# Kernel tuning notes

Hardware: AMD Instinct MI355X
Metric: run time of the kernel (lower is better)

Reference implementation:

```python
import jax, jax.numpy as jnp
import numpy as np

N = 20000      # num_nodes
E = 320000     # num_edges (avg degree 16)
HID = 256      # hid_dim
H = 4          # attention heads
D = HID // H   # per-head dim (concat heads -> HID)
L = 2          # nGAT_layer
OUT = 12       # out_dim / pred_len (decoder steps)
NEG_SLOPE = 0.2


def setup_inputs() -> dict:
    key = jax.random.key(0)
    ks = jax.random.split(key, 16)
    s = 0.05
    nrm = lambda k, shape: jax.random.normal(k, shape, jnp.float32) * s
    return dict(
        x=nrm(ks[0], (N, HID)),
        edge_index=jax.random.randint(ks[1], (2, E), 0, N, dtype=jnp.int32),
        # GATv2Conv params per layer (stacked over L layers)
        gat_w_src=nrm(ks[2], (L, HID, H * D)),
        gat_w_dst=nrm(ks[3], (L, HID, H * D)),
        gat_att=nrm(ks[4], (L, H, D)),
        gat_bias=nrm(ks[5], (L, H * D)),
        # decoder_mlp: Linear(1 + HID -> HID)
        mlp_w=nrm(ks[6], (HID, 1 + HID)),
        mlp_b=nrm(ks[7], (HID,)),
        # nn.LSTM (1 layer, input HID, hidden HID), torch gate order i,f,g,o
        lstm_w_ih=nrm(ks[8], (4 * HID, HID)),
        lstm_w_hh=nrm(ks[9], (4 * HID, HID)),
        lstm_b_ih=nrm(ks[10], (4 * HID,)),
        lstm_b_hh=nrm(ks[11], (4 * HID,)),
        # decoder_init_proj: Linear(HID -> 1); decoder_output_proj: Linear(HID -> 1)
        init_w=nrm(ks[12], (1, HID)),
        init_b=nrm(ks[13], (1,)),
        out_w=nrm(ks[14], (1, HID)),
        out_b=nrm(ks[15], (1,)),
    )


def _gatv2_layer(x, src, dst, w_src, w_dst, att, bias):
    n = x.shape[0]
    xl = (x @ w_src).reshape(n, H, D)   # source-side projection
    xr = (x @ w_dst).reshape(n, H, D)   # destination-side projection
    # GATv2: e_ij = a^T LeakyReLU(Wl x_j + Wr x_i)
    e = jax.nn.leaky_relu(xl[src] + xr[dst], NEG_SLOPE)        # [E,H,D]
    logits = jnp.einsum('ehd,hd->eh', e, att)                   # [E,H]
    # edge softmax over incoming edges of each destination node
    m = jax.ops.segment_max(logits, dst, num_segments=n)        # [N,H]
    ex = jnp.exp(logits - m[dst])
    denom = jax.ops.segment_sum(ex, dst, num_segments=n)
    alpha = ex / denom[dst]                                     # [E,H]
    out = jax.ops.segment_sum(xl[src] * alpha[:, :, None], dst, num_segments=n)
    return out.reshape(n, H * D) + bias


def reference(x, edge_index, gat_w_src, gat_w_dst, gat_att, gat_bias,
              mlp_w, mlp_b, lstm_w_ih, lstm_w_hh, lstm_b_ih, lstm_b_hh,
              init_w, init_b, out_w, out_b):
    src, dst = edge_index[0], edge_index[1]
    # stacked GAT blocks: GATv2Conv + ELU (element == 2)
    for l in range(L):
        x = _gatv2_layer(x, src, dst, gat_w_src[l], gat_w_dst[l], gat_att[l], gat_bias[l])
        x = jax.nn.elu(x)
    # recurrent LSTM decoder, batch = nodes, seq step by step
    ctx = x                      # encoder_context
    h = x                        # h_0 = x (num_layers = 1)
    c = jnp.zeros_like(x)        # c_0 = 0
    prev = x @ init_w.T + init_b  # [N,1]
    outs = []
    for _ in range(OUT):
        dec_in = jnp.concatenate([prev, ctx], axis=1) @ mlp_w.T + mlp_b  # [N,HID]
        gates = dec_in @ lstm_w_ih.T + lstm_b_ih + h @ lstm_w_hh.T + lstm_b_hh
        i_g, f_g, g_g, o_g = jnp.split(gates, 4, axis=1)
        i_g = jax.nn.sigmoid(i_g)
        f_g = jax.nn.sigmoid(f_g)
        o_g = jax.nn.sigmoid(o_g)
        g_g = jnp.tanh(g_g)
        c = f_g * c + i_g * g_g
        h = o_g * jnp.tanh(c)
        prev = h @ out_w.T + out_b  # [N,1]
        outs.append(prev)
    return jnp.concatenate(outs, axis=1)  # [N, OUT]
```

## Files before the change

kernel.cpp:

```cpp
#include <hip/hip_runtime.h>
#include <hip/hip_bf16.h>

#define NN 20000
#define NE 320000
#define TOUT 12
#define DEGMAX 96
#define MR 32
#define NBLK 625

typedef __bf16 bf16x8 __attribute__((ext_vector_type(8)));
typedef float float4v __attribute__((ext_vector_type(4)));

#define LD8(p) (*(const bf16x8*)(p))
#define MFMA16(a,b,c) __builtin_amdgcn_mfma_f32_16x16x32_bf16((a),(b),(c),0,0,0)

__device__ __forceinline__ float bf2f(const __hip_bfloat16 v){ return __bfloat162float(v); }
__device__ __forceinline__ __hip_bfloat16 f2bf(float v){ return __float2bfloat16(v); }
__device__ __forceinline__ float sigmoidr_(float x){ return __builtin_amdgcn_rcpf(1.f + __expf(-x)); }
__device__ __forceinline__ float tanhr_(float x){ return 1.f - 2.f*__builtin_amdgcn_rcpf(__expf(2.f*x) + 1.f); }
__device__ __forceinline__ float rdf(const void* p, int i, int f32){
  return f32 ? ((const float*)p)[i] : __bfloat162float(((const __hip_bfloat16*)p)[i]);
}

__global__ void k_detect(const void* xraw, int* flag){
  __shared__ int cnt;
  if(threadIdx.x == 0) cnt = 0;
  __syncthreads();
  const unsigned* w = (const unsigned*)xraw;
  int local = 0;
  for(int i = threadIdx.x; i < 4096; i += 256){
    unsigned b = (w[i] >> 8) & 0x7F;
    if(b >= 0x33 && b <= 0x3F) local++;
  }
  atomicAdd(&cnt, local);
  __syncthreads();
  if(threadIdx.x == 0) *flag = (cnt > 2048) ? 0 : 1;
}

__global__ void k_fail(float* out, int n){
  int i = blockIdx.x*256 + threadIdx.x;
  if(i < n) out[i] = 256.0f;
}

__global__ void k_count(const int* __restrict__ dst, int* __restrict__ deg){
  int e = blockIdx.x*256 + threadIdx.x;
  if(e < NE){
    unsigned d = (unsigned)dst[e];
    if(d < NN) atomicAdd(&deg[d], 1);
  }
}

__global__ void k_scan(const int* __restrict__ deg, int* __restrict__ offp, int* __restrict__ cursor){
  __shared__ int part[256];
  __shared__ int excl[257];
  const int CH = (NN + 255)/256;
  int tid = threadIdx.x;
  int lo = tid*CH;
  int hi = lo + CH; if(hi > NN) hi = NN;
  int s = 0;
  for(int i=lo;i<hi;i++) s += deg[i];
  part[tid] = s;
  __syncthreads();
  if(tid == 0){
    int run = 0;
    for(int i=0;i<256;i++){ excl[i] = run; run += part[i]; }
    excl[256] = run;
  }
  __syncthreads();
  int run = excl[tid];
  for(int i=lo;i<hi;i++){ offp[i] = run; cursor[i] = run; run += deg[i]; }
  if(tid == 0) offp[NN] = excl[256];
}

__global__ void k_fill(const int* __restrict__ src, const int* __restrict__ dst,
                       int* __restrict__ cursor, int* __restrict__ csr_src){
  int e = blockIdx.x*256 + threadIdx.x;
  if(e >= NE) return;
  unsigned d = (unsigned)dst[e];
  if(d >= NN) return;
  unsigned p = (unsigned)atomicAdd(&cursor[d], 1);
  if(p < NE){
    unsigned sv = (unsigned)src[e];
    csr_src[p] = (sv < NN) ? (int)sv : 0;
  }
}

__global__ void k_prep(const void* __restrict__ w_src, const void* __restrict__ w_dst,
                       const void* __restrict__ w_hh, const void* __restrict__ wih,
                       const void* __restrict__ mlp_w, const int* __restrict__ flag,
                       __hip_bfloat16* __restrict__ wsrcT, __hip_bfloat16* __restrict__ wdstT,
                       __hip_bfloat16* __restrict__ whhp, __hip_bfloat16* __restrict__ wihb,
                       __hip_bfloat16* __restrict__ mlpT){
  int tid = blockIdx.x*256 + threadIdx.x;
  int f = *flag;
  if(tid < 131072){
    int l = tid >> 16, r = tid & 65535, o = r >> 8, i = r & 255;
    wsrcT[tid] = f2bf(rdf(w_src, l*65536 + i*256 + o, f));
    wdstT[tid] = f2bf(rdf(w_dst, l*65536 + i*256 + o, f));
  }
  if(tid < 262144){
    whhp[tid] = f2bf(rdf(w_hh, tid, f));
    wihb[tid] = f2bf(rdf(wih, tid, f));
  }
  if(tid < 65536){
    int k = tid >> 8, j = tid & 255;
    mlpT[tid] = f2bf(rdf(mlp_w, j*257 + 1 + k, f));
  }
}

__global__ void k_prep_ub(const void* __restrict__ wih, const void* __restrict__ mlp_w,
                          const void* __restrict__ mlp_b,
                          const void* __restrict__ b_ih, const void* __restrict__ b_hh,
                          const void* __restrict__ att, const void* __restrict__ gbias,
                          const void* __restrict__ init_w, const void* __restrict__ init_b,
                          const void* __restrict__ out_w, const void* __restrict__ out_b,
                          const int* __restrict__ flag,
                          float* __restrict__ u, float* __restrict__ bc,
                          float* __restrict__ attf, float* __restrict__ gbiasf,
                          float* __restrict__ initwf, float* __restrict__ outwf,
                          float* __restrict__ sc){
  __shared__ float su[256], sb[256];
  int g = blockIdx.x, j = threadIdx.x, f = *flag;
  float w = rdf(wih, g*256 + j, f);
  su[j] = w * rdf(mlp_w, j*257, f);
  sb[j] = w * rdf(mlp_b, j, f);
  if(g < 2){
    int i = g*256 + j;
    attf[i] = rdf(att, i, f);
    gbiasf[i] = rdf(gbias, i, f);
  }
  if(g == 0){
    initwf[j] = rdf(init_w, j, f);
    outwf[j]  = rdf(out_w, j, f);
    if(j == 0){ sc[0] = rdf(init_b, 0, f); sc[1] = rdf(out_b, 0, f); }
  }
  __syncthreads();
  for(int s=128; s>0; s>>=1){
    if(j < s){ su[j] += su[j+s]; sb[j] += sb[j+s]; }
    __syncthreads();
  }
  if(j == 0){ u[g] = su[0]; bc[g] = sb[0] + rdf(b_ih, g, f) + rdf(b_hh, g, f); }
}

__global__ void k_fold(const __hip_bfloat16* __restrict__ whh_pl,
                       const float* __restrict__ u_vec, const float* __restrict__ outwf,
                       __hip_bfloat16* __restrict__ whh2_pl){
  int i = blockIdx.x*256 + threadIdx.x;
  whh2_pl[i] = f2bf(bf2f(whh_pl[i]) + u_vec[i >> 8]*outwf[i & 255]);
}

__global__ void k_pack3(const __hip_bfloat16* __restrict__ Wpl, const __hip_bfloat16* __restrict__ W2pl,
                        const __hip_bfloat16* __restrict__ Wcpl,
                        __hip_bfloat16* __restrict__ WhhP, __hip_bfloat16* __restrict__ Whh2P,
                        __hip_bfloat16* __restrict__ WcP){
  int idx = blockIdx.x*256 + threadIdx.x;
  if(idx >= 32768) return;
  int P    = idx >> 14;
  int cs   = (idx >> 11) & 7;
  int kidx = (idx >> 8) & 7;
  int ntl  = (idx >> 6) & 3;
  int lane = idx & 63;
  int l16 = lane & 15, quad = lane >> 4;
  int brow = ntl*256 + P*128 + cs*16 + l16;
  int srcofs = brow*256 + kidx*32 + quad*8;
  int dst = idx*8;
  *(bf16x8*)(WhhP + dst)  = LD8(Wpl + srcofs);
  *(bf16x8*)(Whh2P + dst) = LD8(W2pl + srcofs);
  *(bf16x8*)(WcP + dst)   = LD8(Wcpl + srcofs);
}

__global__ void k_pack2(const __hip_bfloat16* __restrict__ wsrcT,
                        const __hip_bfloat16* __restrict__ wdstT,
                        __hip_bfloat16* __restrict__ wprojP){
  int idx = blockIdx.x*256 + threadIdx.x;
  if(idx >= 32768) return;
  int m = idx >> 13;
  int fi = idx & 8191;
  int l = m >> 1, role = m & 1;
  int kidx = fi >> 10;
  int nt = (fi >> 6) & 15;
  int lane = fi & 63;
  int l16 = lane & 15, quad = lane >> 4;
  const __hip_bfloat16* src = (role ? wdstT : wsrcT) + l*65536;
  int srcofs = (nt*16 + l16)*256 + kidx*32 + quad*8;
  *(bf16x8*)(wprojP + (size_t)m*65536 + fi*8) = LD8(src + srcofs);
}

__global__ __launch_bounds__(256) void k_gemm_nt_bf(const __hip_bfloat16* __restrict__ A,
                                                    const __hip_bfloat16* __restrict__ B,
                                                    __hip_bfloat16* __restrict__ Cb, int M){
  int wave = threadIdx.x >> 6;
  int lane = threadIdx.x & 63;
  int l16 = lane & 15, quad = lane >> 4, quad8 = quad*8;
  int mBase = blockIdx.x*64 + wave*16;
  int nBase = blockIdx.y*64;
  int arow = mBase + l16; if(arow >= M) arow = M-1;
  const __hip_bfloat16* aptr = A + (size_t)arow*256 + quad8;
  float4v acc[4];
  #pragma unroll
  for(int nt=0;nt<4;nt++){ acc[nt][0]=0.f; acc[nt][1]=0.f; acc[nt][2]=0.f; acc[nt][3]=0.f; }
  for(int k0=0;k0<256;k0+=32){
    bf16x8 a = LD8(aptr + k0);
    #pragma unroll
    for(int nt=0;nt<4;nt++){
      const __hip_bfloat16* bptr = B + (size_t)(nBase + nt*16 + l16)*256 + k0 + quad8;
      acc[nt] = MFMA16(a, LD8(bptr), acc[nt]);
    }
  }
  #pragma unroll
  for(int nt=0;nt<4;nt++){
    int col = nBase + nt*16 + l16;
    #pragma unroll
    for(int r=0;r<4;r++){
      int row = mBase + quad*4 + r;
      if(row < M) Cb[(size_t)row*256 + col] = f2bf(acc[nt][r]);
    }
  }
}

__global__ __launch_bounds__(512, 2) void k_gemm_dual(__hip_bfloat16* __restrict__ P,
                                                      const void* __restrict__ xraw,
                                                      const int* __restrict__ flag,
                                                      int layer0,
                                                      const __hip_bfloat16* __restrict__ BsrcP,
                                                      const __hip_bfloat16* __restrict__ BdstP,
                                                      __hip_bfloat16* __restrict__ Q){
  __shared__ __hip_bfloat16 sA[64*264];
  int tid = threadIdx.x;
  int mBase = blockIdx.x*64;
  {
    int r = tid >> 3;
    int c0 = (tid & 7)*32;
    int grow = mBase + r; if(grow >= NN) grow = NN-1;
    if(layer0){
      int f = *flag;
      #pragma unroll
      for(int j=0;j<32;j++) sA[r*264 + c0 + j] = f2bf(rdf(xraw, grow*256 + c0 + j, f));
    }else{
      const __hip_bfloat16* srcp = P + (size_t)grow*256 + c0;
      #pragma unroll
      for(int j=0;j<4;j++) *(bf16x8*)(&sA[r*264 + c0 + j*8]) = LD8(srcp + j*8);
    }
  }
  __syncthreads();
  int w8 = tid >> 6;
  int w = w8 & 3;
  int role = w8 >> 2;
  int lane = tid&63, l16 = lane&15, quad = lane>>4, quad8 = quad*8;
  const __hip_bfloat16* B = role ? BdstP : BsrcP;
  __hip_bfloat16* C = role ? P : Q;
  const __hip_bfloat16* arow = &sA[(w*16 + l16)*264 + quad8];
  float4v acc[16];
  #pragma unroll
  for(int nt=0;nt<16;nt++){ acc[nt][0]=0.f; acc[nt][1]=0.f; acc[nt][2]=0.f; acc[nt][3]=0.f; }
  for(int kidx=0;kidx<8;kidx++){
    bf16x8 a = *(const bf16x8*)(arow + kidx*32);
    const __hip_bfloat16* bbase = B + (kidx<<13) + (lane<<3);
    #pragma unroll
    for(int nt=0;nt<16;nt++)
      acc[nt] = MFMA16(a, LD8(bbase + (nt<<9)), acc[nt]);
  }
  #pragma unroll
  for(int nt=0;nt<16;nt++){
    int col = nt*16 + l16;
    #pragma unroll
    for(int r=0;r<4;r++){
      int row = mBase + w*16 + quad*4 + r;
      if(row < NN) C[(size_t)row*256 + col] = f2bf(acc[nt][r]);
    }
  }
}

__global__ __launch_bounds__(256) void k_node_fused(const __hip_bfloat16* __restrict__ Q,
                                                    __hip_bfloat16* __restrict__ P,
                                                    const int* __restrict__ offp,
                                                    const int* __restrict__ csr_src,
                                                    const float* __restrict__ attf,
                                                    const float* __restrict__ gbiasf){
  __shared__ float slog[DEGMAX*4];
  __shared__ int ssrc[DEGMAX];
  int node = blockIdx.x;
  int tid = threadIdx.x;
  int s0 = offp[node], s1 = offp[node+1];
  if(s0 < 0) s0 = 0; if(s0 > NE) s0 = NE;
  if(s1 < s0) s1 = s0; if(s1 > NE) s1 = NE;
  int deg = s1 - s0; if(deg > DEGMAX) deg = DEGMAX;
  if(tid < deg){
    unsigned sv = (unsigned)csr_src[s0 + tid];
    ssrc[tid] = (sv < NN) ? (int)sv : 0;
  }
  __syncthreads();
  int w = tid>>6, lane = tid&63;
  int eSlot = lane>>4, li = lane&15;
  float prl[16], attl[16];
  #pragma unroll
  for(int h=0;h<4;h++)
    #pragma unroll
    for(int j=0;j<4;j++){
      int d = h*64 + j*16 + li;
      prl[h*4+j]  = bf2f(P[(size_t)node*256 + d]);
      attl[h*4+j] = attf[d];
    }
  for(int base=0; base<deg; base+=16){
    int e = base + w*4 + eSlot;
    bool valid = (e < deg);
    const __hip_bfloat16* pl = Q + (size_t)ssrc[valid ? e : 0]*256;
    float part[4];
    #pragma unroll
    for(int h=0;h<4;h++){
      float p = 0.f;
      #pragma unroll
      for(int j=0;j<4;j++){
        int d = h*64 + j*16 + li;
        float v = bf2f(pl[d]) + prl[h*4+j];
        v = (v > 0.f) ? v : 0.2f*v;
        p += v * attl[h*4+j];
      }
      part[h] = p;
    }
    #pragma unroll
    for(int h=0;h<4;h++){
      part[h] += __shfl_xor(part[h], 1, 64);
      part[h] += __shfl_xor(part[h], 2, 64);
      part[h] += __shfl_xor(part[h], 4, 64);
      part[h] += __shfl_xor(part[h], 8, 64);
    }
    if(li == 0 && valid){
      #pragma unroll
      for(int h=0;h<4;h++) slog[e*4+h] = part[h];
    }
  }
  __syncthreads();
  {
    int hh = tid >> 6;
    int li64 = tid & 63;
    float m = -1e30f;
    for(int i=li64; i<deg; i+=64) m = fmaxf(m, slog[i*4+hh]);
    #pragma unroll
    for(int s=1; s<64; s<<=1) m = fmaxf(m, __shfl_xor(m, s, 64));
    float den = 0.f;
    for(int i=li64; i<deg; i+=64) den += __expf(slog[i*4+hh] - m);
    #pragma unroll
    for(int s=1; s<64; s<<=1) den += __shfl_xor(den, s, 64);
    float inv = (den > 0.f) ? 1.f/den : 0.f;
    for(int i=li64; i<deg; i+=64) slog[i*4+hh] = __expf(slog[i*4+hh] - m)*inv;
  }
  __syncthreads();
  int d = tid, hd = d>>6;
  float acc = 0.f;
  for(int i=0;i<deg;i++) acc += slog[i*4+hd] * bf2f(Q[(size_t)ssrc[i]*256 + d]);
  acc += gbiasf[d];
  acc = (acc > 0.f) ? acc : (__expf(acc) - 1.f);
  P[(size_t)node*256 + d] = f2bf(acc);
}

__global__ __launch_bounds__(512, 4) void k_lstm32(const __hip_bfloat16* __restrict__ ctx,
                                                   const __hip_bfloat16* __restrict__ WcP,
                                                   const __hip_bfloat16* __restrict__ WhhP,
                                                   const __hip_bfloat16* __restrict__ Whh2P,
                                                   const float* __restrict__ u_vec,
                                                   const float* __restrict__ bc_vec,
                                                   const float* __restrict__ initwf,
                                                   const float* __restrict__ outwf,
                                                   const float* __restrict__ sc,
                                                   float* __restrict__ out){
  __shared__ __hip_bfloat16 sgx[4*4096];
  __shared__ __hip_bfloat16 sh[MR*264];
  __shared__ float spartw[2][MR*16];
  __shared__ float sprev0[MR];
  float* spart = (float*)sgx;
  int tid = threadIdx.x;
  int mBase = blockIdx.x*MR;
  int cs = tid>>6, lane = tid&63, l16 = lane&15, quad = lane>>4, quad8 = quad*8;
  int phase = blockIdx.x & 7;
  int j0 = cs*16 + l16;
  int j1 = 128 + j0;
  {
    int r = tid >> 4;
    int c0 = (tid & 15)*16;
    const __hip_bfloat16* srcp = ctx + (size_t)(mBase + r)*256 + c0;
    *(bf16x8*)(&sh[r*264 + c0])     = LD8(srcp);
    *(bf16x8*)(&sh[r*264 + c0 + 8]) = LD8(srcp + 8);
  }
  __syncthreads();
  {
    int r = tid >> 4;
    int c0 = (tid & 15)*16;
    float part = 0.f;
    #pragma unroll
    for(int j=0;j<16;j++) part += bf2f(sh[r*264 + c0 + j]) * initwf[c0 + j];
    spart[tid] = part;
    __syncthreads();
    if(tid < MR){
      float s = 0.f;
      #pragma unroll
      for(int j=0;j<16;j++) s += spart[tid*16 + j];
      sprev0[tid] = s + sc[0];
    }
    __syncthreads();
  }
  float ow0 = outwf[j0], ow1 = outwf[j1];
  float outb = sc[1];
  bf16x8 gg0, gg1, gg2, gg3;
  {
    float bcl[8];
    #pragma unroll
    for(int g=0;g<4;g++){
      bcl[g]   = bc_vec[g*256 + j0] + u_vec[g*256 + j0]*outb;
      bcl[4+g] = bc_vec[g*256 + j1] + u_vec[g*256 + j1]*outb;
    }
    #pragma unroll
    for(int P2=0;P2<2;P2++){
      float4v acc[8];
      #pragma unroll
      for(int nt=0;nt<8;nt++){ acc[nt][0]=0.f; acc[nt][1]=0.f; acc[nt][2]=0.f; acc[nt][3]=0.f; }
      #pragma unroll 2
      for(int ki=0;ki<8;ki++){
        int kidx = (ki + phase) & 7;
        int k0 = kidx*32;
        bf16x8 a0 = *(const bf16x8*)(&sh[l16*264 + k0 + quad8]);
        bf16x8 a1 = *(const bf16x8*)(&sh[(16 + l16)*264 + k0 + quad8]);
        const __hip_bfloat16* bbase = WcP + P2*131072 + (((cs<<3) + kidx)<<11) + (lane<<3);
        #pragma unroll
        for(int ntl=0;ntl<4;ntl++){
          bf16x8 b = LD8(bbase + (ntl<<9));
          acc[ntl]   = MFMA16(a0, b, acc[ntl]);
          acc[4+ntl] = MFMA16(a1, b, acc[4+ntl]);
        }
      }
      #pragma unroll
      for(int rt=0;rt<2;rt++)
        #pragma unroll
        for(int half=0;half<2;half++){
          bf16x8 v;
          #pragma unroll
          for(int rr=0;rr<2;rr++)
            #pragma unroll
            for(int g=0;g<4;g++){
              int r = half*2 + rr;
              v[rr*4+g] = (__bf16)f2bf(acc[rt*4 + g][r] + bcl[P2*4+g]);
            }
          const int cp = rt*2 + half;
          if(P2 == 0) *(bf16x8*)(&sgx[cp*4096 + tid*8]) = v;
          else if(cp == 0) gg0 = v;
          else if(cp == 1) gg1 = v;
          else if(cp == 2) gg2 = v;
          else             gg3 = v;
        }
    }
  }
  float creg[16];
  #pragma unroll
  for(int i=0;i<16;i++) creg[i] = 0.f;
  #pragma unroll 1
  for(int step=0; step<TOUT; step++){
    const __hip_bfloat16* W = (step == 0) ? WhhP : Whh2P;
    int sb = step & 1;
    float4v acc[8];
    #pragma unroll
    for(int nt=0;nt<8;nt++){ acc[nt][0]=0.f; acc[nt][1]=0.f; acc[nt][2]=0.f; acc[nt][3]=0.f; }
    #pragma unroll 2
    for(int ki=0;ki<8;ki++){
      int kidx = (ki + phase) & 7;
      int k0 = kidx*32;
      bf16x8 a0 = *(const bf16x8*)(&sh[l16*264 + k0 + quad8]);
      bf16x8 a1 = *(const bf16x8*)(&sh[(16 + l16)*264 + k0 + quad8]);
      const __hip_bfloat16* bbase = W + (((cs<<3) + kidx)<<11) + (lane<<3);
      #pragma unroll
      for(int ntl=0;ntl<4;ntl++){
        bf16x8 b = LD8(bbase + (ntl<<9));
        acc[ntl]   = MFMA16(a0, b, acc[ntl]);
        acc[4+ntl] = MFMA16(a1, b, acc[4+ntl]);
      }
    }
    float hA[8];
    #pragma unroll
    for(int rt=0; rt<2; rt++){
      bf16x8 ga = *(const bf16x8*)(&sgx[(rt*2)*4096 + tid*8]);
      bf16x8 gb = *(const bf16x8*)(&sgx[(rt*2+1)*4096 + tid*8]);
      float hsum[4];
      #pragma unroll
      for(int r=0;r<4;r++){
        int row = rt*16 + quad*4 + r;
        int jb = (r&1)*4;
        float gx0, gx1, gx2, gx3;
        if(r < 2){
          gx0 = bf2f((__hip_bfloat16)ga[jb]);   gx1 = bf2f((__hip_bfloat16)ga[jb+1]);
          gx2 = bf2f((__hip_bfloat16)ga[jb+2]); gx3 = bf2f((__hip_bfloat16)ga[jb+3]);
        }else{
          gx0 = bf2f((__hip_bfloat16)gb[jb]);   gx1 = bf2f((__hip_bfloat16)gb[jb+1]);
          gx2 = bf2f((__hip_bfloat16)gb[jb+2]); gx3 = bf2f((__hip_bfloat16)gb[jb+3]);
        }
        float g0 = acc[rt*4 + 0][r] + gx0;
        float g1 = acc[rt*4 + 1][r] + gx1;
        float g2 = acc[rt*4 + 2][r] + gx2;
        float g3 = acc[rt*4 + 3][r] + gx3;
        if(step == 0){
          float pd = sprev0[row] - outb;
          g0 += pd*u_vec[j0];
          g1 += pd*u_vec[256 + j0];
          g2 += pd*u_vec[512 + j0];
          g3 += pd*u_vec[768 + j0];
        }
        float iv = sigmoidr_(g0), fv = sigmoidr_(g1);
        float gv = tanhr_(g2),    ov = sigmoidr_(g3);
        float cn = fv*creg[rt*4 + r] + iv*gv;
        creg[rt*4 + r] = cn;
        float hn = ov * tanhr_(cn);
        hA[rt*4 + r] = hn;
        hsum[r] = hn * ow0;
      }
      #pragma unroll
      for(int r=0;r<4;r++){
        hsum[r] += __shfl_xor(hsum[r], 1, 64);
        hsum[r] += __shfl_xor(hsum[r], 2, 64);
        hsum[r] += __shfl_xor(hsum[r], 4, 64);
        hsum[r] += __shfl_xor(hsum[r], 8, 64);
      }
      if(l16 == 0){
        #pragma unroll
        for(int r=0;r<4;r++)
          spartw[sb][(rt*16 + quad*4 + r)*16 + cs*2] = hsum[r];
      }
    }
    #pragma unroll
    for(int nt=0;nt<8;nt++){ acc[nt][0]=0.f; acc[nt][1]=0.f; acc[nt][2]=0.f; acc[nt][3]=0.f; }
    #pragma unroll 2
    for(int ki=0;ki<8;ki++){
      int kidx = (ki + phase) & 7;
      int k0 = kidx*32;
      bf16x8 a0 = *(const bf16x8*)(&sh[l16*264 + k0 + quad8]);
      bf16x8 a1 = *(const bf16x8*)(&sh[(16 + l16)*264 + k0 + quad8]);
      const __hip_bfloat16* bbase = W + 131072 + (((cs<<3) + kidx)<<11) + (lane<<3);
      #pragma unroll
      for(int ntl=0;ntl<4;ntl++){
        bf16x8 b = LD8(bbase + (ntl<<9));
        acc[ntl]   = MFMA16(a0, b, acc[ntl]);
        acc[4+ntl] = MFMA16(a1, b, acc[4+ntl]);
      }
    }
    __syncthreads();
    #pragma unroll
    for(int rt=0; rt<2; rt++){
      bf16x8 ga = (rt == 0) ? gg0 : gg2;
      bf16x8 gb = (rt == 0) ? gg1 : gg3;
      float hsum[4];
      #pragma unroll
      for(int r=0;r<4;r++){
        int row = rt*16 + quad*4 + r;
        int jb = (r&1)*4;
        float gx0, gx1, gx2, gx3;
        if(r < 2){
          gx0 = bf2f((__hip_bfloat16)ga[jb]);   gx1 = bf2f((__hip_bfloat16)ga[jb+1]);
          gx2 = bf2f((__hip_bfloat16)ga[jb+2]); gx3 = bf2f((__hip_bfloat16)ga[jb+3]);
        }else{
          gx0 = bf2f((__hip_bfloat16)gb[jb]);   gx1 = bf2f((__hip_bfloat16)gb[jb+1]);
          gx2 = bf2f((__hip_bfloat16)gb[jb+2]); gx3 = bf2f((__hip_bfloat16)gb[jb+3]);
        }
        float g0 = acc[rt*4 + 0][r] + gx0;
        float g1 = acc[rt*4 + 1][r] + gx1;
        float g2 = acc[rt*4 + 2][r] + gx2;
        float g3 = acc[rt*4 + 3][r] + gx3;
        if(step == 0){
          float pd = sprev0[row] - outb;
          g0 += pd*u_vec[j1];
          g1 += pd*u_vec[256 + j1];
          g2 += pd*u_vec[512 + j1];
          g3 += pd*u_vec[768 + j1];
        }
        float iv = sigmoidr_(g0), fv = sigmoidr_(g1);
        float gv = tanhr_(g2),    ov = sigmoidr_(g3);
        float cn = fv*creg[8 + rt*4 + r] + iv*gv;
        creg[8 + rt*4 + r] = cn;
        float hn = ov * tanhr_(cn);
        sh[row*264 + j0] = f2bf(hA[rt*4 + r]);
        sh[row*264 + j1] = f2bf(hn);
        hsum[r] = hn * ow1;
      }
      #pragma unroll
      for(int r=0;r<4;r++){
        hsum[r] += __shfl_xor(hsum[r], 1, 64);
        hsum[r] += __shfl_xor(hsum[r], 2, 64);
        hsum[r] += __shfl_xor(hsum[r], 4, 64);
        hsum[r] += __shfl_xor(hsum[r], 8, 64);
      }
      if(l16 == 0){
        #pragma unroll
        for(int r=0;r<4;r++)
          spartw[sb][(rt*16 + quad*4 + r)*16 + cs*2 + 1] = hsum[r];
      }
    }
    __syncthreads();
    if(tid < MR){
      float s = outb;
      #pragma unroll
      for(int c=0;c<16;c++) s += spartw[sb][tid*16 + c];
      out[(size_t)(mBase + tid)*TOUT + step] = s;
    }
  }
}

extern "C" void kernel_launch(void* const* d_in, const int* in_sizes, int n_in,
                              void* d_out, int out_size, void* d_ws, size_t ws_size,
                              hipStream_t stream){
  const void* x      = d_in[0];
  const int*  ei     = (const int*)d_in[1];
  const void* w_src  = d_in[2];
  const void* w_dst  = d_in[3];
  const void* att    = d_in[4];
  const void* gbias  = d_in[5];
  const void* mlp_w  = d_in[6];
  const void* mlp_b  = d_in[7];
  const void* w_ih   = d_in[8];
  const void* w_hh   = d_in[9];
  const void* b_ih   = d_in[10];
  const void* b_hh   = d_in[11];
  const void* init_w = d_in[12];
  const void* init_b = d_in[13];
  const void* out_w  = d_in[14];
  const void* out_b  = d_in[15];
  float* out = (float*)d_out;
  const int* srcp = ei;
  const int* dstp = ei + NE;
  (void)in_sizes; (void)n_in;

  char* ws = (char*)d_ws;
  size_t off = 0;
  auto alloc = [&](size_t bytes)->void*{
    void* p = ws + off;
    off += (bytes + 255) & ~(size_t)255;
    return p;
  };
  __hip_bfloat16* P = (__hip_bfloat16*)alloc((size_t)NN*256*2);
  __hip_bfloat16* Q = (__hip_bfloat16*)alloc((size_t)NN*256*2);
  int* deg      = (int*)alloc((size_t)NN*4);
  int* offp     = (int*)alloc((size_t)(NN+1)*4);
  int* cursor   = (int*)alloc((size_t)NN*4);
  int* csr_src  = (int*)alloc((size_t)NE*4);
  __hip_bfloat16* wsrcT   = (__hip_bfloat16*)alloc((size_t)131072*2);
  __hip_bfloat16* wdstT   = (__hip_bfloat16*)alloc((size_t)131072*2);
  __hip_bfloat16* wprojP  = (__hip_bfloat16*)alloc((size_t)4*65536*2);
  __hip_bfloat16* whh_pl  = (__hip_bfloat16*)alloc((size_t)262144*2);
  __hip_bfloat16* whh2_pl = (__hip_bfloat16*)alloc((size_t)262144*2);
  __hip_bfloat16* Wc_pl   = (__hip_bfloat16*)alloc((size_t)262144*2);
  __hip_bfloat16* WhhP    = (__hip_bfloat16*)alloc((size_t)262144*2);
  __hip_bfloat16* Whh2P   = (__hip_bfloat16*)alloc((size_t)262144*2);
  __hip_bfloat16* WcP     = (__hip_bfloat16*)alloc((size_t)262144*2);
  __hip_bfloat16* wihb    = (__hip_bfloat16*)alloc((size_t)262144*2);
  __hip_bfloat16* mlpT    = (__hip_bfloat16*)alloc((size_t)65536*2);
  float* u_vec  = (float*)alloc(1024*4);
  float* bc_vec = (float*)alloc(1024*4);
  float* attf   = (float*)alloc(512*4);
  float* gbiasf = (float*)alloc(512*4);
  float* initwf = (float*)alloc(256*4);
  float* outwf  = (float*)alloc(256*4);
  float* sc     = (float*)alloc(2*4);
  int*   flag   = (int*)alloc(4);

  if(off > ws_size){
    k_fail<<<(out_size + 255)/256, 256, 0, stream>>>(out, out_size);
    return;
  }

  k_detect<<<1, 256, 0, stream>>>(x, flag);
  hipMemsetAsync(deg, 0, (size_t)NN*4, stream);
  hipMemsetAsync(csr_src, 0xFF, (size_t)NE*4, stream);
  k_count<<<NE/256, 256, 0, stream>>>(dstp, deg);
  k_scan<<<1, 256, 0, stream>>>(deg, offp, cursor);
  k_fill<<<NE/256, 256, 0, stream>>>(srcp, dstp, cursor, csr_src);
  k_prep<<<1024, 256, 0, stream>>>(w_src, w_dst, w_hh, w_ih, mlp_w, flag,
                                   wsrcT, wdstT, whh_pl, wihb, mlpT);
  k_prep_ub<<<1024, 256, 0, stream>>>(w_ih, mlp_w, mlp_b, b_ih, b_hh, att, gbias,
                                      init_w, init_b, out_w, out_b, flag,
                                      u_vec, bc_vec, attf, gbiasf, initwf, outwf, sc);
  {
    dim3 gwc(16, 4);
    k_gemm_nt_bf<<<gwc, 256, 0, stream>>>(wihb, mlpT, Wc_pl, 1024);
  }
  k_fold<<<1024, 256, 0, stream>>>(whh_pl, u_vec, outwf, whh2_pl);
  k_pack3<<<128, 256, 0, stream>>>(whh_pl, whh2_pl, Wc_pl, WhhP, Whh2P, WcP);
  k_pack2<<<128, 256, 0, stream>>>(wsrcT, wdstT, wprojP);

  for(int l=0;l<2;l++){
    k_gemm_dual<<<313, 512, 0, stream>>>(P, x, flag, (l == 0) ? 1 : 0,
                                         wprojP + (size_t)(l*2)*65536,
                                         wprojP + (size_t)(l*2+1)*65536, Q);
    k_node_fused<<<NN, 256, 0, stream>>>(Q, P, offp, csr_src, attf + l*256, gbiasf + l*256);
  }

  k_lstm32<<<NBLK, 512, 0, stream>>>(P, WcP, WhhP, Whh2P, u_vec, bc_vec,
                                     initwf, outwf, sc, out);
}
```

Measured before the change: 730.2 us.

## Enlarge LSTM row tile to 80 with 1024-thread blocks; vectorize GAT logit loads

```diff
diff --git a/kernel.cpp b/kernel.cpp
--- a/kernel.cpp
+++ b/kernel.cpp
@@ -5,8 +5,8 @@
 #define NE 320000
 #define TOUT 12
 #define DEGMAX 96
-#define MR 32
-#define NBLK 625
+#define MR 80
+#define NBLK 250
 
 typedef __bf16 bf16x8 __attribute__((ext_vector_type(8)));
 typedef float float4v __attribute__((ext_vector_type(4)));
@@ -293,42 +293,29 @@
   int w = tid>>6, lane = tid&63;
   int eSlot = lane>>4, li = lane&15;
   float prl[16], attl[16];
-  #pragma unroll
-  for(int h=0;h<4;h++)
-    #pragma unroll
-    for(int j=0;j<4;j++){
-      int d = h*64 + j*16 + li;
-      prl[h*4+j]  = bf2f(P[(size_t)node*256 + d]);
-      attl[h*4+j] = attf[d];
-    }
+  {
+    const __hip_bfloat16* prow = P + (size_t)node*256 + li*16;
+    bf16x8 p0 = LD8(prow), p1 = LD8(prow + 8);
+    #pragma unroll
+    for(int j=0;j<8;j++){ prl[j] = bf2f((__hip_bfloat16)p0[j]); prl[8+j] = bf2f((__hip_bfloat16)p1[j]); }
+    #pragma unroll
+    for(int j=0;j<16;j++) attl[j] = attf[li*16 + j];
+  }
   for(int base=0; base<deg; base+=16){
     int e = base + w*4 + eSlot;
     bool valid = (e < deg);
-    const __hip_bfloat16* pl = Q + (size_t)ssrc[valid ? e : 0]*256;
-    float part[4];
-    #pragma unroll
-    for(int h=0;h<4;h++){
-      float p = 0.f;
-      #pragma unroll
-      for(int j=0;j<4;j++){
-        int d = h*64 + j*16 + li;
-        float v = bf2f(pl[d]) + prl[h*4+j];
-        v = (v > 0.f) ? v : 0.2f*v;
-        p += v * attl[h*4+j];
-      }
-      part[h] = p;
-    }
-    #pragma unroll
-    for(int h=0;h<4;h++){
-      part[h] += __shfl_xor(part[h], 1, 64);
-      part[h] += __shfl_xor(part[h], 2, 64);
-      part[h] += __shfl_xor(part[h], 4, 64);
-      part[h] += __shfl_xor(part[h], 8, 64);
-    }
-    if(li == 0 && valid){
-      #pragma unroll
-      for(int h=0;h<4;h++) slog[e*4+h] = part[h];
-    }
+    const __hip_bfloat16* qrow = Q + (size_t)ssrc[valid ? e : 0]*256 + li*16;
+    bf16x8 q0 = LD8(qrow), q1 = LD8(qrow + 8);
+    float part = 0.f;
+    #pragma unroll
+    for(int j=0;j<16;j++){
+      float v = bf2f((__hip_bfloat16)(j<8 ? q0[j] : q1[j-8])) + prl[j];
+      v = (v > 0.f) ? v : 0.2f*v;
+      part += v * attl[j];
+    }
+    part += __shfl_xor(part, 1, 64);
+    part += __shfl_xor(part, 2, 64);
+    if((li & 3) == 0 && valid) slog[e*4 + (li>>2)] = part;
   }
   __syncthreads();
   {
@@ -354,33 +341,40 @@
   P[(size_t)node*256 + d] = f2bf(acc);
 }
 
-__global__ __launch_bounds__(512, 4) void k_lstm32(const __hip_bfloat16* __restrict__ ctx,
-                                                   const __hip_bfloat16* __restrict__ WcP,
-                                                   const __hip_bfloat16* __restrict__ WhhP,
-                                                   const __hip_bfloat16* __restrict__ Whh2P,
-                                                   const float* __restrict__ u_vec,
-                                                   const float* __restrict__ bc_vec,
-                                                   const float* __restrict__ initwf,
-                                                   const float* __restrict__ outwf,
-                                                   const float* __restrict__ sc,
-                                                   float* __restrict__ out){
-  __shared__ __hip_bfloat16 sgx[4*4096];
+__global__ __launch_bounds__(1024, 4) void k_lstm80(const __hip_bfloat16* __restrict__ ctx,
+                                                    const __hip_bfloat16* __restrict__ WcP,
+                                                    const __hip_bfloat16* __restrict__ WhhP,
+                                                    const __hip_bfloat16* __restrict__ Whh2P,
+                                                    const float* __restrict__ u_vec,
+                                                    const float* __restrict__ bc_vec,
+                                                    const float* __restrict__ initwf,
+                                                    const float* __restrict__ outwf,
+                                                    const float* __restrict__ sc,
+                                                    float* __restrict__ out){
+  __shared__ __hip_bfloat16 sgx[6*8192];
   __shared__ __hip_bfloat16 sh[MR*264];
   __shared__ float spartw[2][MR*16];
   __shared__ float sprev0[MR];
   float* spart = (float*)sgx;
   int tid = threadIdx.x;
   int mBase = blockIdx.x*MR;
-  int cs = tid>>6, lane = tid&63, l16 = lane&15, quad = lane>>4, quad8 = quad*8;
+  int w = tid>>6, lane = tid&63, l16 = lane&15, quad = lane>>4, quad8 = quad*8;
   int phase = blockIdx.x & 7;
-  int j0 = cs*16 + l16;
-  int j1 = 128 + j0;
+  int j = (w>>3)*128 + (w&7)*16 + l16;
+  const size_t wofs = (size_t)(w>>3)*131072;
+  const int csw = w & 7;
   {
     int r = tid >> 4;
     int c0 = (tid & 15)*16;
     const __hip_bfloat16* srcp = ctx + (size_t)(mBase + r)*256 + c0;
     *(bf16x8*)(&sh[r*264 + c0])     = LD8(srcp);
     *(bf16x8*)(&sh[r*264 + c0 + 8]) = LD8(srcp + 8);
+    if(tid < 256){
+      int r2 = 64 + (tid >> 4);
+      const __hip_bfloat16* s2 = ctx + (size_t)(mBase + r2)*256 + c0;
+      *(bf16x8*)(&sh[r2*264 + c0])     = LD8(s2);
+      *(bf16x8*)(&sh[r2*264 + c0 + 8]) = LD8(s2 + 8);
+    }
   }
   __syncthreads();
   {
@@ -388,48 +382,61 @@
     int c0 = (tid & 15)*16;
     float part = 0.f;
     #pragma unroll
-    for(int j=0;j<16;j++) part += bf2f(sh[r*264 + c0 + j]) * initwf[c0 + j];
+    for(int jj=0;jj<16;jj++) part += bf2f(sh[r*264 + c0 + jj]) * initwf[c0 + jj];
     spart[tid] = part;
     __syncthreads();
-    if(tid < MR){
+    if(tid < 64){
       float s = 0.f;
       #pragma unroll
-      for(int j=0;j<16;j++) s += spart[tid*16 + j];
+      for(int jj=0;jj<16;jj++) s += spart[tid*16 + jj];
       sprev0[tid] = s + sc[0];
     }
     __syncthreads();
-  }
-  float ow0 = outwf[j0], ow1 = outwf[j1];
+    float part2 = 0.f;
+    if(tid < 256){
+      int r2 = 64 + (tid >> 4);
+      #pragma unroll
+      for(int jj=0;jj<16;jj++) part2 += bf2f(sh[r2*264 + c0 + jj]) * initwf[c0 + jj];
+    }
+    spart[tid] = part2;
+    __syncthreads();
+    if(tid < 16){
+      float s = 0.f;
+      #pragma unroll
+      for(int jj=0;jj<16;jj++) s += spart[tid*16 + jj];
+      sprev0[64 + tid] = s + sc[0];
+    }
+    __syncthreads();
+  }
+  float ow = outwf[j];
   float outb = sc[1];
   bf16x8 gg0, gg1, gg2, gg3;
   {
-    float bcl[8];
-    #pragma unroll
-    for(int g=0;g<4;g++){
-      bcl[g]   = bc_vec[g*256 + j0] + u_vec[g*256 + j0]*outb;
-      bcl[4+g] = bc_vec[g*256 + j1] + u_vec[g*256 + j1]*outb;
-    }
-    #pragma unroll
-    for(int P2=0;P2<2;P2++){
-      float4v acc[8];
-      #pragma unroll
-      for(int nt=0;nt<8;nt++){ acc[nt][0]=0.f; acc[nt][1]=0.f; acc[nt][2]=0.f; acc[nt][3]=0.f; }
+    float bcl[4];
+    #pragma unroll
+    for(int g=0;g<4;g++) bcl[g] = bc_vec[g*256 + j] + u_vec[g*256 + j]*outb;
+    {
+      float4v acc[12];
+      #pragma unroll
+      for(int nt=0;nt<12;nt++){ acc[nt][0]=0.f; acc[nt][1]=0.f; acc[nt][2]=0.f; acc[nt][3]=0.f; }
       #pragma unroll 2
       for(int ki=0;ki<8;ki++){
         int kidx = (ki + phase) & 7;
         int k0 = kidx*32;
         bf16x8 a0 = *(const bf16x8*)(&sh[l16*264 + k0 + quad8]);
         bf16x8 a1 = *(const bf16x8*)(&sh[(16 + l16)*264 + k0 + quad8]);
-        const __hip_bfloat16* bbase = WcP + P2*131072 + (((cs<<3) + kidx)<<11) + (lane<<3);
+        bf16x8 a2 = *(const bf16x8*)(&sh[(32 + l16)*264 + k0 + quad8]);
+        const __hip_bfloat16* bbase = WcP + wofs + (((csw<<3) + kidx)<<11) + (lane<<3);
         #pragma unroll
         for(int ntl=0;ntl<4;ntl++){
           bf16x8 b = LD8(bbase + (ntl<<9));
           acc[ntl]   = MFMA16(a0, b, acc[ntl]);
           acc[4+ntl] = MFMA16(a1, b, acc[4+ntl]);
+          acc[8+ntl] = MFMA16(a2, b, acc[8+ntl]);
         }
       }
       #pragma unroll
-      for(int rt=0;rt<2;rt++)
+      for(int rt=0;rt<3;rt++)
         #pragma unroll
         for(int half=0;half<2;half++){
           bf16x8 v;
@@ -438,46 +445,81 @@
             #pragma unroll
             for(int g=0;g<4;g++){
               int r = half*2 + rr;
-              v[rr*4+g] = (__bf16)f2bf(acc[rt*4 + g][r] + bcl[P2*4+g]);
+              v[rr*4+g] = (__bf16)f2bf(acc[rt*4 + g][r] + bcl[g]);
             }
           const int cp = rt*2 + half;
-          if(P2 == 0) *(bf16x8*)(&sgx[cp*4096 + tid*8]) = v;
-          else if(cp == 0) gg0 = v;
-          else if(cp == 1) gg1 = v;
-          else if(cp == 2) gg2 = v;
+          *(bf16x8*)(&sgx[cp*8192 + tid*8]) = v;
+        }
+    }
+    {
+      float4v acc[8];
+      #pragma unroll
+      for(int nt=0;nt<8;nt++){ acc[nt][0]=0.f; acc[nt][1]=0.f; acc[nt][2]=0.f; acc[nt][3]=0.f; }
+      #pragma unroll 2
+      for(int ki=0;ki<8;ki++){
+        int kidx = (ki + phase) & 7;
+        int k0 = kidx*32;
+        bf16x8 a3 = *(const bf16x8*)(&sh[(48 + l16)*264 + k0 + quad8]);
+        bf16x8 a4 = *(const bf16x8*)(&sh[(64 + l16)*264 + k0 + quad8]);
+        const __hip_bfloat16* bbase = WcP + wofs + (((csw<<3) + kidx)<<11) + (lane<<3);
+        #pragma unroll
+        for(int ntl=0;ntl<4;ntl++){
+          bf16x8 b = LD8(bbase + (ntl<<9));
+          acc[ntl]   = MFMA16(a3, b, acc[ntl]);
+          acc[4+ntl] = MFMA16(a4, b, acc[4+ntl]);
+        }
+      }
+      #pragma unroll
+      for(int rtl=0;rtl<2;rtl++)
+        #pragma unroll
+        for(int half=0;half<2;half++){
+          bf16x8 v;
+          #pragma unroll
+          for(int rr=0;rr<2;rr++)
+            #pragma unroll
+            for(int g=0;g<4;g++){
+              int r = half*2 + rr;
+              v[rr*4+g] = (__bf16)f2bf(acc[rtl*4 + g][r] + bcl[g]);
+            }
+          const int cp = 6 + rtl*2 + half;
+          if(cp == 6)      gg0 = v;
+          else if(cp == 7) gg1 = v;
+          else if(cp == 8) gg2 = v;
           else             gg3 = v;
         }
     }
   }
-  float creg[16];
+  float creg[20];
   #pragma unroll
-  for(int i=0;i<16;i++) creg[i] = 0.f;
+  for(int i=0;i<20;i++) creg[i] = 0.f;
   #pragma unroll 1
   for(int step=0; step<TOUT; step++){
-    const __hip_bfloat16* W = (step == 0) ? WhhP : Whh2P;
+    const __hip_bfloat16* Wb = ((step == 0) ? WhhP : Whh2P) + wofs;
     int sb = step & 1;
-    float4v acc[8];
-    #pragma unroll
-    for(int nt=0;nt<8;nt++){ acc[nt][0]=0.f; acc[nt][1]=0.f; acc[nt][2]=0.f; acc[nt][3]=0.f; }
+    float4v acc1[12];
+    #pragma unroll
+    for(int nt=0;nt<12;nt++){ acc1[nt][0]=0.f; acc1[nt][1]=0.f; acc1[nt][2]=0.f; acc1[nt][3]=0.f; }
     #pragma unroll 2
     for(int ki=0;ki<8;ki++){
       int kidx = (ki + phase) & 7;
       int k0 = kidx*32;
       bf16x8 a0 = *(const bf16x8*)(&sh[l16*264 + k0 + quad8]);
       bf16x8 a1 = *(const bf16x8*)(&sh[(16 + l16)*264 + k0 + quad8]);
-      const __hip_bfloat16* bbase = W + (((cs<<3) + kidx)<<11) + (lane<<3);
+      bf16x8 a2 = *(const bf16x8*)(&sh[(32 + l16)*264 + k0 + quad8]);
+      const __hip_bfloat16* bbase = Wb + (((csw<<3) + kidx)<<11) + (lane<<3);
       #pragma unroll
       for(int ntl=0;ntl<4;ntl++){
         bf16x8 b = LD8(bbase + (ntl<<9));
-        acc[ntl]   = MFMA16(a0, b, acc[ntl]);
-        acc[4+ntl] = MFMA16(a1, b, acc[4+ntl]);
-      }
-    }
-    float hA[8];
-    #pragma unroll
-    for(int rt=0; rt<2; rt++){
-      bf16x8 ga = *(const bf16x8*)(&sgx[(rt*2)*4096 + tid*8]);
-      bf16x8 gb = *(const bf16x8*)(&sgx[(rt*2+1)*4096 + tid*8]);
+        acc1[ntl]   = MFMA16(a0, b, acc1[ntl]);
+        acc1[4+ntl] = MFMA16(a1, b, acc1[4+ntl]);
+        acc1[8+ntl] = MFMA16(a2, b, acc1[8+ntl]);
+      }
+    }
+    __syncthreads();
+    #pragma unroll
+    for(int rt=0; rt<3; rt++){
+      bf16x8 ga = *(const bf16x8*)(&sgx[(rt*2)*8192 + tid*8]);
+      bf16x8 gb = *(const bf16x8*)(&sgx[(rt*2+1)*8192 + tid*8]);
       float hsum[4];
       #pragma unroll
       for(int r=0;r<4;r++){
@@ -491,24 +533,24 @@
           gx0 = bf2f((__hip_bfloat16)gb[jb]);   gx1 = bf2f((__hip_bfloat16)gb[jb+1]);
           gx2 = bf2f((__hip_bfloat16)gb[jb+2]); gx3 = bf2f((__hip_bfloat16)gb[jb+3]);
         }
-        float g0 = acc[rt*4 + 0][r] + gx0;
-        float g1 = acc[rt*4 + 1][r] + gx1;
-        float g2 = acc[rt*4 + 2][r] + gx2;
-        float g3 = acc[rt*4 + 3][r] + gx3;
+        float g0 = acc1[rt*4 + 0][r] + gx0;
+        float g1 = acc1[rt*4 + 1][r] + gx1;
+        float g2 = acc1[rt*4 + 2][r] + gx2;
+        float g3 = acc1[rt*4 + 3][r] + gx3;
         if(step == 0){
           float pd = sprev0[row] - outb;
-          g0 += pd*u_vec[j0];
-          g1 += pd*u_vec[256 + j0];
-          g2 += pd*u_vec[512 + j0];
-          g3 += pd*u_vec[768 + j0];
+          g0 += pd*u_vec[j];
+          g1 += pd*u_vec[256 + j];
+          g2 += pd*u_vec[512 + j];
+          g3 += pd*u_vec[768 + j];
         }
         float iv = sigmoidr_(g0), fv = sigmoidr_(g1);
         float gv = tanhr_(g2),    ov = sigmoidr_(g3);
         float cn = fv*creg[rt*4 + r] + iv*gv;
         creg[rt*4 + r] = cn;
         float hn = ov * tanhr_(cn);
-        hA[rt*4 + r] = hn;
-        hsum[r] = hn * ow0;
+        sh[row*264 + j] = f2bf(hn);
+        hsum[r] = hn * ow;
       }
       #pragma unroll
       for(int r=0;r<4;r++){
@@ -520,30 +562,32 @@
       if(l16 == 0){
         #pragma unroll
         for(int r=0;r<4;r++)
-          spartw[sb][(rt*16 + quad*4 + r)*16 + cs*2] = hsum[r];
-      }
-    }
-    #pragma unroll
-    for(int nt=0;nt<8;nt++){ acc[nt][0]=0.f; acc[nt][1]=0.f; acc[nt][2]=0.f; acc[nt][3]=0.f; }
+          spartw[sb][(rt*16 + quad*4 + r)*16 + w] = hsum[r];
+      }
+    }
+    float4v acc2[8];
+    #pragma unroll
+    for(int nt=0;nt<8;nt++){ acc2[nt][0]=0.f; acc2[nt][1]=0.f; acc2[nt][2]=0.f; acc2[nt][3]=0.f; }
     #pragma unroll 2
     for(int ki=0;ki<8;ki++){
       int kidx = (ki + phase) & 7;
       int k0 = kidx*32;
-      bf16x8 a0 = *(const bf16x8*)(&sh[l16*264 + k0 + quad8]);
-      bf16x8 a1 = *(const bf16x8*)(&sh[(16 + l16)*264 + k0 + quad8]);
-      const __hip_bfloat16* bbase = W + 131072 + (((cs<<3) + kidx)<<11) + (lane<<3);
+      bf16x8 a3 = *(const bf16x8*)(&sh[(48 + l16)*264 + k0 + quad8]);
+      bf16x8 a4 = *(const bf16x8*)(&sh[(64 + l16)*264 + k0 + quad8]);
+      const __hip_bfloat16* bbase = Wb + (((csw<<3) + kidx)<<11) + (lane<<3);
       #pragma unroll
       for(int ntl=0;ntl<4;ntl++){
         bf16x8 b = LD8(bbase + (ntl<<9));
-        acc[ntl]   = MFMA16(a0, b, acc[ntl]);
-        acc[4+ntl] = MFMA16(a1, b, acc[4+ntl]);
+        acc2[ntl]   = MFMA16(a3, b, acc2[ntl]);
+        acc2[4+ntl] = MFMA16(a4, b, acc2[4+ntl]);
       }
     }
     __syncthreads();
     #pragma unroll
-    for(int rt=0; rt<2; rt++){
-      bf16x8 ga = (rt == 0) ? gg0 : gg2;
-      bf16x8 gb = (rt == 0) ? gg1 : gg3;
+    for(int rtl=0; rtl<2; rtl++){
+      const int rt = 3 + rtl;
+      bf16x8 ga = (rtl == 0) ? gg0 : gg2;
+      bf16x8 gb = (rtl == 0) ? gg1 : gg3;
       float hsum[4];
       #pragma unroll
       for(int r=0;r<4;r++){
@@ -557,25 +601,24 @@
           gx0 = bf2f((__hip_bfloat16)gb[jb]);   gx1 = bf2f((__hip_bfloat16)gb[jb+1]);
           gx2 = bf2f((__hip_bfloat16)gb[jb+2]); gx3 = bf2f((__hip_bfloat16)gb[jb+3]);
         }
-        float g0 = acc[rt*4 + 0][r] + gx0;
-        float g1 = acc[rt*4 + 1][r] + gx1;
-        float g2 = acc[rt*4 + 2][r] + gx2;
-        float g3 = acc[rt*4 + 3][r] + gx3;
+        float g0 = acc2[rtl*4 + 0][r] + gx0;
+        float g1 = acc2[rtl*4 + 1][r] + gx1;
+        float g2 = acc2[rtl*4 + 2][r] + gx2;
+        float g3 = acc2[rtl*4 + 3][r] + gx3;
         if(step == 0){
           float pd = sprev0[row] - outb;
-          g0 += pd*u_vec[j1];
-          g1 += pd*u_vec[256 + j1];
-          g2 += pd*u_vec[512 + j1];
-          g3 += pd*u_vec[768 + j1];
+          g0 += pd*u_vec[j];
+          g1 += pd*u_vec[256 + j];
+          g2 += pd*u_vec[512 + j];
+          g3 += pd*u_vec[768 + j];
         }
         float iv = sigmoidr_(g0), fv = sigmoidr_(g1);
         float gv = tanhr_(g2),    ov = sigmoidr_(g3);
-        float cn = fv*creg[8 + rt*4 + r] + iv*gv;
-        creg[8 + rt*4 + r] = cn;
+        float cn = fv*creg[rt*4 + r] + iv*gv;
+        creg[rt*4 + r] = cn;
         float hn = ov * tanhr_(cn);
-        sh[row*264 + j0] = f2bf(hA[rt*4 + r]);
-        sh[row*264 + j1] = f2bf(hn);
-        hsum[r] = hn * ow1;
+        sh[row*264 + j] = f2bf(hn);
+        hsum[r] = hn * ow;
       }
       #pragma unroll
       for(int r=0;r<4;r++){
@@ -587,7 +630,7 @@
       if(l16 == 0){
         #pragma unroll
         for(int r=0;r<4;r++)
-          spartw[sb][(rt*16 + quad*4 + r)*16 + cs*2 + 1] = hsum[r];
+          spartw[sb][(rt*16 + quad*4 + r)*16 + w] = hsum[r];
       }
     }
     __syncthreads();
@@ -688,6 +731,6 @@
     k_node_fused<<<NN, 256, 0, stream>>>(Q, P, offp, csr_src, attf + l*256, gbiasf + l*256);
   }
 
-  k_lstm32<<<NBLK, 512, 0, stream>>>(P, WcP, WhhP, Whh2P, u_vec, bc_vec,
-                                     initwf, outwf, sc, out);
-}
+  k_lstm80<<<NBLK, 1024, 0, stream>>>(P, WcP, WhhP, Whh2P, u_vec, bc_vec,
+                                      initwf, outwf, sc, out);
+}
```

New measurement: 706.5 us. -3.3%, faster.
